# Optimization experiments

Hardware: AMD Instinct MI355X
Metric: run time of the kernel (lower is better)

## Reference

```python
import jax, jax.numpy as jnp
import numpy as np
import math

H = 8  # num_heads

def setup_inputs() -> dict:
    key = jax.random.key(0)
    ks = jax.random.split(key, 12)
    B, N, M, k = 2, 8192, 8192, 32
    dq, dk, dv = 256, 256, 256
    s = 1.0 / math.sqrt(dq)
    inp = {
        'Q': jax.random.normal(ks[0], (B, N, dq), dtype=jnp.float32),
        'K': jax.random.normal(ks[1], (B, M, dk), dtype=jnp.float32),
        'neighbours': jax.random.randint(ks[2], (B, N, k), 0, M),
        'Wq': jax.random.normal(ks[3], (dq, dv), dtype=jnp.float32) * s,
        'bq': jnp.zeros((dv,), dtype=jnp.float32),
        'Wk': jax.random.normal(ks[4], (dk, dv), dtype=jnp.float32) * s,
        'bk': jnp.zeros((dv,), dtype=jnp.float32),
        'Wv': jax.random.normal(ks[5], (dk, dv), dtype=jnp.float32) * s,
        'bv': jnp.zeros((dv,), dtype=jnp.float32),
        'Wo': jax.random.normal(ks[6], (dv, dv), dtype=jnp.float32) * (1.0 / math.sqrt(dv)),
        'bo': jnp.zeros((dv,), dtype=jnp.float32),
    }
    return inp

def reference(Q, K, neighbours, Wq, bq, Wk, bk, Wv, bv, Wo, bo):
    B, N, _ = Q.shape
    dv = Wq.shape[1]
    ds = dv // H
    # project and split heads (contiguous channel chunks == reshape)
    Qh = (Q @ Wq + bq).reshape(B, N, H, ds)            # [B,N,H,ds]
    Kh = (K @ Wk + bk).reshape(B, -1, H, ds)           # [B,M,H,ds]
    Vh = (K @ Wv + bv).reshape(B, -1, H, ds)           # [B,M,H,ds]
    # gather per-node kNN neighbour keys/values: [B,N,k,H,ds]
    gather = jax.vmap(lambda x, idx: x[idx])
    Kn = gather(Kh, neighbours)
    Vn = gather(Vh, neighbours)
    # scale uses full latent size (faithful to original), not head dim
    scale = 1.0 / math.sqrt(dv)
    E = jnp.einsum('bnhd,bnkhd->bnhk', Qh, Kn) * scale  # [B,N,H,k]
    A = jax.nn.softmax(E, axis=-1)
    AV = jnp.einsum('bnhk,bnkhd->bnhd', A, Vn).reshape(B, N, dv)
    return AV @ Wo + bo
```

## Files before the change

kernel.cpp:

```cpp
#include <hip/hip_runtime.h>
#include <hip/hip_bf16.h>
#include <stdint.h>

typedef unsigned short u16;
typedef __attribute__((ext_vector_type(8))) short short8;
typedef __attribute__((ext_vector_type(4))) float f32x4;

__device__ __forceinline__ u16 f2bf(float f) {
    union { float f; unsigned int i; } v; v.f = f;
    unsigned int b = v.i;
    return (u16)((b + 0x7FFFu + ((b >> 16) & 1u)) >> 16);
}

__device__ __forceinline__ short8 cvt8(float4 a, float4 b) {
    union { __hip_bfloat162 h[4]; short8 s; } u;
    u.h[0] = __float22bfloat162_rn(make_float2(a.x, a.y));
    u.h[1] = __float22bfloat162_rn(make_float2(a.z, a.w));
    u.h[2] = __float22bfloat162_rn(make_float2(b.x, b.y));
    u.h[3] = __float22bfloat162_rn(make_float2(b.z, b.w));
    return u.s;
}

typedef const __attribute__((address_space(1))) void* as1cv;
typedef __attribute__((address_space(3))) void* as3v;
__device__ __forceinline__ void gload16(const void* g, void* l) {
    __builtin_amdgcn_global_load_lds((as1cv)g, (as3v)l, 16, 0, 0);
}

__device__ __forceinline__ void up2(unsigned int v, float& lo, float& hi) {
    union { unsigned int i; float f; } a, b;
    a.i = v << 16; b.i = v & 0xffff0000u;
    lo = a.f; hi = b.f;
}

__global__ __launch_bounds__(256) void wprep(
    const float* __restrict__ W0, const float* __restrict__ W1,
    const float* __restrict__ W2, const float* __restrict__ W3,
    u16* __restrict__ T0, u16* __restrict__ T1,
    u16* __restrict__ T2, u16* __restrict__ T3)
{
    const float* W = blockIdx.z == 0 ? W0 : blockIdx.z == 1 ? W1 : blockIdx.z == 2 ? W2 : W3;
    u16*        T  = blockIdx.z == 0 ? T0 : blockIdx.z == 1 ? T1 : blockIdx.z == 2 ? T2 : T3;
    __shared__ u16 ts[64][65];
    int k0 = blockIdx.x * 64, n0 = blockIdx.y * 64;
    int t = threadIdx.x;
    int r = t >> 2, cq = (t & 3) * 16;
    const float4* src = reinterpret_cast<const float4*>(W + (k0 + r) * 256 + n0 + cq);
    for (int u = 0; u < 4; ++u) {
        float4 v = src[u];
        int c = cq + u * 4;
        ts[r][c + 0] = f2bf(v.x); ts[r][c + 1] = f2bf(v.y);
        ts[r][c + 2] = f2bf(v.z); ts[r][c + 3] = f2bf(v.w);
    }
    __syncthreads();
    u16* dst = T + (n0 + r) * 256 + k0 + cq;
    for (int u = 0; u < 16; ++u) dst[u] = ts[cq + u][r];
}

__global__ __launch_bounds__(256) void gemm_proj(
    const float* __restrict__ Q, const float* __restrict__ K,
    const u16* __restrict__ Wtq, const u16* __restrict__ Wtk, const u16* __restrict__ Wtv,
    const float* __restrict__ bq, const float* __restrict__ bk, const float* __restrict__ bv,
    u16* __restrict__ Qh, u16* __restrict__ Kh, u16* __restrict__ Vh)
{
    int z = blockIdx.z;
    const float* Af   = (z == 0) ? Q   : K;
    const u16*   Wt   = (z == 0) ? Wtq : (z == 1) ? Wtk : Wtv;
    const float* bias = (z == 0) ? bq  : (z == 1) ? bk  : bv;
    u16*         C    = (z == 0) ? Qh  : (z == 1) ? Kh  : Vh;

    __shared__ float Asf[128 * 64];
    __shared__ u16   Bs[128 * 64];

    int t = threadIdx.x;
    int lane = t & 63, w = t >> 6;
    int row0 = blockIdx.x * 128, col0 = blockIdx.y * 128;
    int wr = (w >> 1) * 64, wc = (w & 1) * 64;
    int qd = lane >> 4, md = lane & 15;

    f32x4 acc[4][4] = {};

    for (int kt = 0; kt < 256; kt += 64) {
#pragma unroll
        for (int u = 0; u < 8; ++u) {
            int chunk = w * 8 + u;
            int s = chunk * 64 + lane;
            int r = s >> 4, c = s & 15;
            gload16(Af + (size_t)(row0 + r) * 256 + kt + ((c ^ (r & 15)) * 4),
                    (char*)Asf + chunk * 1024);
        }
#pragma unroll
        for (int u = 0; u < 4; ++u) {
            int chunk = w * 4 + u;
            int s = chunk * 64 + lane;
            int r = s >> 3, c = s & 7;
            gload16(Wt + (size_t)(col0 + r) * 256 + kt + ((c ^ (r & 7)) * 8),
                    (char*)Bs + chunk * 1024);
        }
        __syncthreads();
#pragma unroll
        for (int ks = 0; ks < 64; ks += 32) {
            short8 af[4], bf[4];
#pragma unroll
            for (int i = 0; i < 4; ++i) {
                int ar = wr + i * 16 + md;
                int c0 = (ks >> 2) + qd * 2;
                int x = ar & 15;
                float4 fa0 = reinterpret_cast<const float4*>(Asf)[ar * 16 + (c0 ^ x)];
                float4 fa1 = reinterpret_cast<const float4*>(Asf)[ar * 16 + ((c0 + 1) ^ x)];
                af[i] = cvt8(fa0, fa1);
            }
#pragma unroll
            for (int j = 0; j < 4; ++j) {
                int br = wc + j * 16 + md;
                int slot = ((ks >> 3) + qd) ^ (br & 7);
                bf[j] = reinterpret_cast<const short8*>(Bs)[br * 8 + slot];
            }
#pragma unroll
            for (int i = 0; i < 4; ++i)
#pragma unroll
                for (int j = 0; j < 4; ++j)
                    acc[i][j] = __builtin_amdgcn_mfma_f32_16x16x32_bf16(
                        af[i], bf[j], acc[i][j], 0, 0, 0);
        }
        __syncthreads();
    }

#pragma unroll
    for (int i = 0; i < 4; ++i)
#pragma unroll
        for (int j = 0; j < 4; ++j) {
            int col = col0 + wc + j * 16 + md;
            float b = bias[col];
#pragma unroll
            for (int r = 0; r < 4; ++r) {
                int row = row0 + wr + i * 16 + qd * 4 + r;
                C[(size_t)row * 256 + col] = f2bf(acc[i][j][r] + b);
            }
        }
}

__global__ __launch_bounds__(256) void gemm_out(
    const u16* __restrict__ Ab, const u16* __restrict__ Wt,
    const float* __restrict__ bias, float* __restrict__ Cout)
{
    __shared__ u16 As[64 * 64];
    __shared__ u16 Bs[128 * 64];

    int t = threadIdx.x;
    int lane = t & 63, w = t >> 6;
    int row0 = blockIdx.x * 64, col0 = blockIdx.y * 128;
    int wr = (w >> 1) * 32, wc = (w & 1) * 64;
    int qd = lane >> 4, md = lane & 15;

    f32x4 acc[2][4] = {};

    for (int kt = 0; kt < 256; kt += 64) {
#pragma unroll
        for (int u = 0; u < 2; ++u) {
            int chunk = w * 2 + u;
            int s = chunk * 64 + lane;
            int r = s >> 3, c = s & 7;
            gload16(Ab + (size_t)(row0 + r) * 256 + kt + ((c ^ (r & 7)) * 8),
                    (char*)As + chunk * 1024);
        }
#pragma unroll
        for (int u = 0; u < 4; ++u) {
            int chunk = w * 4 + u;
            int s = chunk * 64 + lane;
            int r = s >> 3, c = s & 7;
            gload16(Wt + (size_t)(col0 + r) * 256 + kt + ((c ^ (r & 7)) * 8),
                    (char*)Bs + chunk * 1024);
        }
        __syncthreads();
#pragma unroll
        for (int ks = 0; ks < 64; ks += 32) {
            short8 af[2], bf[4];
#pragma unroll
            for (int i = 0; i < 2; ++i) {
                int ar = wr + i * 16 + md;
                int slot = ((ks >> 3) + qd) ^ (ar & 7);
                af[i] = reinterpret_cast<const short8*>(As)[ar * 8 + slot];
            }
#pragma unroll
            for (int j = 0; j < 4; ++j) {
                int br = wc + j * 16 + md;
                int slot = ((ks >> 3) + qd) ^ (br & 7);
                bf[j] = reinterpret_cast<const short8*>(Bs)[br * 8 + slot];
            }
#pragma unroll
            for (int i = 0; i < 2; ++i)
#pragma unroll
                for (int j = 0; j < 4; ++j)
                    acc[i][j] = __builtin_amdgcn_mfma_f32_16x16x32_bf16(
                        af[i], bf[j], acc[i][j], 0, 0, 0);
        }
        __syncthreads();
    }

#pragma unroll
    for (int i = 0; i < 2; ++i)
#pragma unroll
        for (int j = 0; j < 4; ++j) {
            int col = col0 + wc + j * 16 + md;
            float b = bias[col];
#pragma unroll
            for (int r = 0; r < 4; ++r) {
                int row = row0 + wr + i * 16 + qd * 4 + r;
                Cout[(size_t)row * 256 + col] = acc[i][j][r] + b;
            }
        }
}

__device__ __forceinline__ int attn_row(int blk, int w) {
    int g = blk & 7;
    int batch = g >> 2;
    int group = (blk >> 3) * 4 + (g & 3);
    return batch * 8192 + group * 4 + w;
}

__global__ __launch_bounds__(256) void attn_score(
    const u16* __restrict__ Qh, const u16* __restrict__ Kh,
    const int* __restrict__ nbr, u16* __restrict__ Wgt)
{
    __shared__ int jbs[4][32];
    __shared__ u16 wsm[4][256];

    int t = threadIdx.x;
    int w = t >> 6, lane = t & 63;
    int row = attn_row(blockIdx.x, w);
    int bbase = (row >> 13) << 13;

    int c8 = lane & 31;
    int jh = lane >> 5;

    if (lane < 32) {
        int ji = nbr[(size_t)row * 32 + lane];
        jbs[w][lane] = (bbase + ji) * 256;
    }

    float qf[8];
    {
        uint4 qw = *reinterpret_cast<const uint4*>(Qh + (size_t)row * 256 + c8 * 8);
        up2(qw.x, qf[0], qf[1]); up2(qw.y, qf[2], qf[3]);
        up2(qw.z, qf[4], qf[5]); up2(qw.w, qf[6], qf[7]);
    }

    float e16[16];
#pragma unroll
    for (int bb = 0; bb < 2; ++bb) {
        uint4 kw[8];
#pragma unroll
        for (int u = 0; u < 8; ++u) {
            int koff = jbs[w][jh * 16 + bb * 8 + u];
            kw[u] = *reinterpret_cast<const uint4*>(Kh + (size_t)koff + c8 * 8);
        }
#pragma unroll
        for (int u = 0; u < 8; ++u) {
            float k0, k1;
            float p = 0.f;
            up2(kw[u].x, k0, k1); p = fmaf(qf[0], k0, p); p = fmaf(qf[1], k1, p);
            up2(kw[u].y, k0, k1); p = fmaf(qf[2], k0, p); p = fmaf(qf[3], k1, p);
            up2(kw[u].z, k0, k1); p = fmaf(qf[4], k0, p); p = fmaf(qf[5], k1, p);
            up2(kw[u].w, k0, k1); p = fmaf(qf[6], k0, p); p = fmaf(qf[7], k1, p);
            p += __shfl_xor(p, 1);
            p += __shfl_xor(p, 2);
            e16[bb * 8 + u] = p * 0.0625f;
        }
    }

    float m = e16[0];
#pragma unroll
    for (int jj = 1; jj < 16; ++jj) m = fmaxf(m, e16[jj]);
    m = fmaxf(m, __shfl_xor(m, 32));
    float s = 0.f;
#pragma unroll
    for (int jj = 0; jj < 16; ++jj) { e16[jj] = __expf(e16[jj] - m); s += e16[jj]; }
    s += __shfl_xor(s, 32);
    float rs = 1.0f / s;

    if ((c8 & 3) == 0) {
        int h = c8 >> 2;
#pragma unroll
        for (int jj = 0; jj < 16; ++jj)
            wsm[w][h * 32 + jh * 16 + jj] = f2bf(e16[jj] * rs);
    }
    __syncthreads();

    {
        uint2 v = *reinterpret_cast<const uint2*>(&wsm[w][lane * 4]);
        *reinterpret_cast<uint2*>(Wgt + (size_t)row * 256 + lane * 4) = v;
    }
}

__global__ __launch_bounds__(256) void attn_av(
    const u16* __restrict__ Vh, const int* __restrict__ nbr,
    const u16* __restrict__ Wgt, u16* __restrict__ AVb)
{
    __shared__ int jbs[4][32];

    int t = threadIdx.x;
    int w = t >> 6, lane = t & 63;
    int row = attn_row(blockIdx.x, w);
    int bbase = (row >> 13) << 13;

    int c8 = lane & 31;
    int jh = lane >> 5;
    int h = c8 >> 2;

    if (lane < 32) {
        int ji = nbr[(size_t)row * 32 + lane];
        jbs[w][lane] = (bbase + ji) * 256;
    }

    float e16[16];
    {
        const uint4* wp = reinterpret_cast<const uint4*>(
            Wgt + (size_t)row * 256 + h * 32 + jh * 16);
        uint4 v = wp[0];
        up2(v.x, e16[0], e16[1]);  up2(v.y, e16[2], e16[3]);
        up2(v.z, e16[4], e16[5]);  up2(v.w, e16[6], e16[7]);
        v = wp[1];
        up2(v.x, e16[8], e16[9]);  up2(v.y, e16[10], e16[11]);
        up2(v.z, e16[12], e16[13]); up2(v.w, e16[14], e16[15]);
    }

    float acc[8] = {};
#pragma unroll
    for (int bb = 0; bb < 2; ++bb) {
        uint4 vv[8];
#pragma unroll
        for (int u = 0; u < 8; ++u) {
            int voff = jbs[w][jh * 16 + bb * 8 + u];
            vv[u] = *reinterpret_cast<const uint4*>(Vh + (size_t)voff + c8 * 8);
        }
#pragma unroll
        for (int u = 0; u < 8; ++u) {
            float v0, v1;
            float wgt = e16[bb * 8 + u];
            up2(vv[u].x, v0, v1); acc[0] = fmaf(wgt, v0, acc[0]); acc[1] = fmaf(wgt, v1, acc[1]);
            up2(vv[u].y, v0, v1); acc[2] = fmaf(wgt, v0, acc[2]); acc[3] = fmaf(wgt, v1, acc[3]);
            up2(vv[u].z, v0, v1); acc[4] = fmaf(wgt, v0, acc[4]); acc[5] = fmaf(wgt, v1, acc[5]);
            up2(vv[u].w, v0, v1); acc[6] = fmaf(wgt, v0, acc[6]); acc[7] = fmaf(wgt, v1, acc[7]);
        }
    }
#pragma unroll
    for (int u = 0; u < 8; ++u) acc[u] += __shfl_xor(acc[u], 32);

    if (lane < 32) {
        union { __hip_bfloat162 h2[4]; uint4 u4; } o;
        o.h2[0] = __float22bfloat162_rn(make_float2(acc[0], acc[1]));
        o.h2[1] = __float22bfloat162_rn(make_float2(acc[2], acc[3]));
        o.h2[2] = __float22bfloat162_rn(make_float2(acc[4], acc[5]));
        o.h2[3] = __float22bfloat162_rn(make_float2(acc[6], acc[7]));
        *reinterpret_cast<uint4*>(AVb + (size_t)row * 256 + c8 * 8) = o.u4;
    }
}

extern "C" void kernel_launch(void* const* d_in, const int* in_sizes, int n_in,
                              void* d_out, int out_size, void* d_ws, size_t ws_size,
                              hipStream_t stream) {
    const float* Q   = (const float*)d_in[0];
    const float* K   = (const float*)d_in[1];
    const int*   nbr = (const int*)d_in[2];
    const float* Wq  = (const float*)d_in[3];
    const float* bq  = (const float*)d_in[4];
    const float* Wk  = (const float*)d_in[5];
    const float* bk  = (const float*)d_in[6];
    const float* Wv  = (const float*)d_in[7];
    const float* bv  = (const float*)d_in[8];
    const float* Wo  = (const float*)d_in[9];
    const float* bo  = (const float*)d_in[10];
    float* out = (float*)d_out;

    char* ws = (char*)d_ws;
    size_t off = 0;
    auto alloc = [&](size_t bytes) -> void* {
        void* p = ws + off;
        off += (bytes + 255) & ~(size_t)255;
        return p;
    };
    const size_t MN = 16384;
    u16* Wtq = (u16*)alloc(256 * 256 * 2);
    u16* Wtk = (u16*)alloc(256 * 256 * 2);
    u16* Wtv = (u16*)alloc(256 * 256 * 2);
    u16* Wto = (u16*)alloc(256 * 256 * 2);
    u16* Qh  = (u16*)alloc(MN * 256 * 2);
    u16* Kh  = (u16*)alloc(MN * 256 * 2);
    u16* Vh  = (u16*)alloc(MN * 256 * 2);
    u16* AVb = (u16*)alloc(MN * 256 * 2);
    u16* Wgt = (u16*)alloc(MN * 256 * 2);

    wprep<<<dim3(4, 4, 4), 256, 0, stream>>>(Wq, Wk, Wv, Wo, Wtq, Wtk, Wtv, Wto);
    gemm_proj<<<dim3(128, 2, 3), 256, 0, stream>>>(Q, K, Wtq, Wtk, Wtv,
                                                   bq, bk, bv, Qh, Kh, Vh);
    attn_score<<<dim3(4096), 256, 0, stream>>>(Qh, Kh, nbr, Wgt);
    attn_av<<<dim3(4096), 256, 0, stream>>>(Vh, nbr, Wgt, AVb);
    gemm_out<<<dim3(256, 2), 256, 0, stream>>>(AVb, Wto, bo, out);
}
```

Before: 152.6 us.

## Retile projection GEMM to full-width columns and split attention rows by head half

The projection GEMM now gives each block 64 rows and all 256 output columns, so the fp32 activation tile is loaded and converted to bf16 once per row block rather than once for each of two column blocks. The attention score and AV kernels now give each wave half of a row's heads (128 channels), doubling the grid. This lowers per-wave register use, lets each wave issue its gathers in one batch, and removes the shared-memory staging and __syncthreads in the score kernel. In exchange there are extra cross-lane shuffle reductions, neighbour indices are loaded twice per row, and the GEMM holds more accumulators per wave.

New measurement: 153.7 us. Within noise of the previous version (+0.7%).

```diff
diff --git a/kernel.cpp b/kernel.cpp
--- a/kernel.cpp
+++ b/kernel.cpp
@@ -69,25 +69,100 @@
     const float* bias = (z == 0) ? bq  : (z == 1) ? bk  : bv;
     u16*         C    = (z == 0) ? Qh  : (z == 1) ? Kh  : Vh;
 
-    __shared__ float Asf[128 * 64];
-    __shared__ u16   Bs[128 * 64];
+    __shared__ float Asf[64 * 64];
+    __shared__ u16   Bs[256 * 64];
 
     int t = threadIdx.x;
     int lane = t & 63, w = t >> 6;
-    int row0 = blockIdx.x * 128, col0 = blockIdx.y * 128;
-    int wr = (w >> 1) * 64, wc = (w & 1) * 64;
+    int row0 = blockIdx.x * 64;
+    int wr = (w >> 1) * 32, wc = (w & 1) * 128;
     int qd = lane >> 4, md = lane & 15;
 
-    f32x4 acc[4][4] = {};
+    f32x4 acc[2][8] = {};
 
     for (int kt = 0; kt < 256; kt += 64) {
 #pragma unroll
-        for (int u = 0; u < 8; ++u) {
-            int chunk = w * 8 + u;
+        for (int u = 0; u < 4; ++u) {
+            int chunk = w * 4 + u;
             int s = chunk * 64 + lane;
             int r = s >> 4, c = s & 15;
             gload16(Af + (size_t)(row0 + r) * 256 + kt + ((c ^ (r & 15)) * 4),
                     (char*)Asf + chunk * 1024);
+        }
+#pragma unroll
+        for (int u = 0; u < 8; ++u) {
+            int chunk = w * 8 + u;
+            int s = chunk * 64 + lane;
+            int r = s >> 3, c = s & 7;
+            gload16(Wt + (size_t)r * 256 + kt + ((c ^ (r & 7)) * 8),
+                    (char*)Bs + chunk * 1024);
+        }
+        __syncthreads();
+#pragma unroll
+        for (int ks = 0; ks < 64; ks += 32) {
+            short8 af[2], bf[8];
+#pragma unroll
+            for (int i = 0; i < 2; ++i) {
+                int ar = wr + i * 16 + md;
+                int c0 = (ks >> 2) + qd * 2;
+                int x = ar & 15;
+                float4 fa0 = reinterpret_cast<const float4*>(Asf)[ar * 16 + (c0 ^ x)];
+                float4 fa1 = reinterpret_cast<const float4*>(Asf)[ar * 16 + ((c0 + 1) ^ x)];
+                af[i] = cvt8(fa0, fa1);
+            }
+#pragma unroll
+            for (int j = 0; j < 8; ++j) {
+                int br = wc + j * 16 + md;
+                int slot = ((ks >> 3) + qd) ^ (br & 7);
+                bf[j] = reinterpret_cast<const short8*>(Bs)[br * 8 + slot];
+            }
+#pragma unroll
+            for (int i = 0; i < 2; ++i)
+#pragma unroll
+                for (int j = 0; j < 8; ++j)
+                    acc[i][j] = __builtin_amdgcn_mfma_f32_16x16x32_bf16(
+                        af[i], bf[j], acc[i][j], 0, 0, 0);
+        }
+        __syncthreads();
+    }
+
+#pragma unroll
+    for (int i = 0; i < 2; ++i)
+#pragma unroll
+        for (int j = 0; j < 8; ++j) {
+            int col = wc + j * 16 + md;
+            float b = bias[col];
+#pragma unroll
+            for (int r = 0; r < 4; ++r) {
+                int row = row0 + wr + i * 16 + qd * 4 + r;
+                C[(size_t)row * 256 + col] = f2bf(acc[i][j][r] + b);
+            }
+        }
+}
+
+__global__ __launch_bounds__(256) void gemm_out(
+    const u16* __restrict__ Ab, const u16* __restrict__ Wt,
+    const float* __restrict__ bias, float* __restrict__ Cout)
+{
+    __shared__ u16 As[64 * 64];
+    __shared__ u16 Bs[128 * 64];
+
+    int t = threadIdx.x;
+    int lane = t & 63, w = t >> 6;
+    int row0 = blockIdx.x * 64, col0 = blockIdx.y * 128;
+    int wr = (w >> 1) * 32, wc = (w & 1) * 64;
+    int qd = lane >> 4, md = lane & 15;
+
+    f32x4 acc[2][4] = {};
+
+    for (int kt = 0; kt < 256; kt += 64) {
+#pragma unroll
+        for (int u = 0; u < 2; ++u) {
+            int chunk = w * 2 + u;
+            int s = chunk * 64 + lane;
+            int r = s >> 3, c = s & 7;
+            gload16(Ab + (size_t)(row0 + r) * 256 + kt + ((c ^ (r & 7)) * 8),
+                    (char*)As + chunk * 1024);
         }
 #pragma unroll
         for (int u = 0; u < 4; ++u) {
@@ -100,15 +175,12 @@
         __syncthreads();
 #pragma unroll
         for (int ks = 0; ks < 64; ks += 32) {
-            short8 af[4], bf[4];
-#pragma unroll
-            for (int i = 0; i < 4; ++i) {
+            short8 af[2], bf[4];
+#pragma unroll
+            for (int i = 0; i < 2; ++i) {
                 int ar = wr + i * 16 + md;
-                int c0 = (ks >> 2) + qd * 2;
-                int x = ar & 15;
-                float4 fa0 = reinterpret_cast<const float4*>(Asf)[ar * 16 + (c0 ^ x)];
-                float4 fa1 = reinterpret_cast<const float4*>(Asf)[ar * 16 + ((c0 + 1) ^ x)];
-                af[i] = cvt8(fa0, fa1);
+                int slot = ((ks >> 3) + qd) ^ (ar & 7);
+                af[i] = reinterpret_cast<const short8*>(As)[ar * 8 + slot];
             }
 #pragma unroll
             for (int j = 0; j < 4; ++j) {
@@ -117,7 +189,7 @@
                 bf[j] = reinterpret_cast<const short8*>(Bs)[br * 8 + slot];
             }
 #pragma unroll
-            for (int i = 0; i < 4; ++i)
+            for (int i = 0; i < 2; ++i)
 #pragma unroll
                 for (int j = 0; j < 4; ++j)
                     acc[i][j] = __builtin_amdgcn_mfma_f32_16x16x32_bf16(
@@ -127,7 +199,7 @@
     }
 
 #pragma unroll
-    for (int i = 0; i < 4; ++i)
+    for (int i = 0; i < 2; ++i)
 #pragma unroll
         for (int j = 0; j < 4; ++j) {
             int col = col0 + wc + j * 16 + md;
@@ -135,88 +207,17 @@
 #pragma unroll
             for (int r = 0; r < 4; ++r) {
                 int row = row0 + wr + i * 16 + qd * 4 + r;
-                C[(size_t)row * 256 + col] = f2bf(acc[i][j][r] + b);
-            }
-        }
-}
-
-__global__ __launch_bounds__(256) void gemm_out(
-    const u16* __restrict__ Ab, const u16* __restrict__ Wt,
-    const float* __restrict__ bias, float* __restrict__ Cout)
-{
-    __shared__ u16 As[64 * 64];
-    __shared__ u16 Bs[128 * 64];
-
-    int t = threadIdx.x;
-    int lane = t & 63, w = t >> 6;
-    int row0 = blockIdx.x * 64, col0 = blockIdx.y * 128;
-    int wr = (w >> 1) * 32, wc = (w & 1) * 64;
-    int qd = lane >> 4, md = lane & 15;
-
-    f32x4 acc[2][4] = {};
-
-    for (int kt = 0; kt < 256; kt += 64) {
-#pragma unroll
-        for (int u = 0; u < 2; ++u) {
-            int chunk = w * 2 + u;
-            int s = chunk * 64 + lane;
-            int r = s >> 3, c = s & 7;
-            gload16(Ab + (size_t)(row0 + r) * 256 + kt + ((c ^ (r & 7)) * 8),
-                    (char*)As + chunk * 1024);
-        }
-#pragma unroll
-        for (int u = 0; u < 4; ++u) {
-            int chunk = w * 4 + u;
-            int s = chunk * 64 + lane;
-            int r = s >> 3, c = s & 7;
-            gload16(Wt + (size_t)(col0 + r) * 256 + kt + ((c ^ (r & 7)) * 8),
-                    (char*)Bs + chunk * 1024);
-        }
-        __syncthreads();
-#pragma unroll
-        for (int ks = 0; ks < 64; ks += 32) {
-            short8 af[2], bf[4];
-#pragma unroll
-            for (int i = 0; i < 2; ++i) {
-                int ar = wr + i * 16 + md;
-                int slot = ((ks >> 3) + qd) ^ (ar & 7);
-                af[i] = reinterpret_cast<const short8*>(As)[ar * 8 + slot];
-            }
-#pragma unroll
-            for (int j = 0; j < 4; ++j) {
-                int br = wc + j * 16 + md;
-                int slot = ((ks >> 3) + qd) ^ (br & 7);
-                bf[j] = reinterpret_cast<const short8*>(Bs)[br * 8 + slot];
-            }
-#pragma unroll
-            for (int i = 0; i < 2; ++i)
-#pragma unroll
-                for (int j = 0; j < 4; ++j)
-                    acc[i][j] = __builtin_amdgcn_mfma_f32_16x16x32_bf16(
-                        af[i], bf[j], acc[i][j], 0, 0, 0);
-        }
-        __syncthreads();
-    }
-
-#pragma unroll
-    for (int i = 0; i < 2; ++i)
-#pragma unroll
-        for (int j = 0; j < 4; ++j) {
-            int col = col0 + wc + j * 16 + md;
-            float b = bias[col];
-#pragma unroll
-            for (int r = 0; r < 4; ++r) {
-                int row = row0 + wr + i * 16 + qd * 4 + r;
                 Cout[(size_t)row * 256 + col] = acc[i][j][r] + b;
             }
         }
 }
 
-__device__ __forceinline__ int attn_row(int blk, int w) {
+__device__ __forceinline__ void attn_map2(int blk, int w, int& row, int& hf) {
     int g = blk & 7;
     int batch = g >> 2;
-    int group = (blk >> 3) * 4 + (g & 3);
-    return batch * 8192 + group * 4 + w;
+    hf = (g >> 1) & 1;
+    int cb = (blk >> 3) * 2 + (g & 1);
+    row = batch * 8192 + cb * 4 + w;
 }
 
 __global__ __launch_bounds__(256) void attn_score(
@@ -224,72 +225,67 @@
     const int* __restrict__ nbr, u16* __restrict__ Wgt)
 {
     __shared__ int jbs[4][32];
-    __shared__ u16 wsm[4][256];
 
     int t = threadIdx.x;
     int w = t >> 6, lane = t & 63;
-    int row = attn_row(blockIdx.x, w);
+    int row, hf;
+    attn_map2(blockIdx.x, w, row, hf);
     int bbase = (row >> 13) << 13;
 
-    int c8 = lane & 31;
-    int jh = lane >> 5;
+    int c4 = lane & 15;
+    int jg = lane >> 4;
 
     if (lane < 32) {
         int ji = nbr[(size_t)row * 32 + lane];
-        jbs[w][lane] = (bbase + ji) * 256;
+        jbs[w][lane] = (bbase + ji) * 256 + hf * 128;
     }
 
     float qf[8];
     {
-        uint4 qw = *reinterpret_cast<const uint4*>(Qh + (size_t)row * 256 + c8 * 8);
+        uint4 qw = *reinterpret_cast<const uint4*>(Qh + (size_t)row * 256 + hf * 128 + c4 * 8);
         up2(qw.x, qf[0], qf[1]); up2(qw.y, qf[2], qf[3]);
         up2(qw.z, qf[4], qf[5]); up2(qw.w, qf[6], qf[7]);
     }
 
-    float e16[16];
-#pragma unroll
-    for (int bb = 0; bb < 2; ++bb) {
-        uint4 kw[8];
-#pragma unroll
-        for (int u = 0; u < 8; ++u) {
-            int koff = jbs[w][jh * 16 + bb * 8 + u];
-            kw[u] = *reinterpret_cast<const uint4*>(Kh + (size_t)koff + c8 * 8);
-        }
-#pragma unroll
-        for (int u = 0; u < 8; ++u) {
-            float k0, k1;
-            float p = 0.f;
-            up2(kw[u].x, k0, k1); p = fmaf(qf[0], k0, p); p = fmaf(qf[1], k1, p);
-            up2(kw[u].y, k0, k1); p = fmaf(qf[2], k0, p); p = fmaf(qf[3], k1, p);
-            up2(kw[u].z, k0, k1); p = fmaf(qf[4], k0, p); p = fmaf(qf[5], k1, p);
-            up2(kw[u].w, k0, k1); p = fmaf(qf[6], k0, p); p = fmaf(qf[7], k1, p);
-            p += __shfl_xor(p, 1);
-            p += __shfl_xor(p, 2);
-            e16[bb * 8 + u] = p * 0.0625f;
-        }
-    }
-
-    float m = e16[0];
-#pragma unroll
-    for (int jj = 1; jj < 16; ++jj) m = fmaxf(m, e16[jj]);
+    uint4 kw[8];
+#pragma unroll
+    for (int u = 0; u < 8; ++u) {
+        int koff = jbs[w][jg * 8 + u];
+        kw[u] = *reinterpret_cast<const uint4*>(Kh + (size_t)koff + c4 * 8);
+    }
+
+    float e8[8];
+#pragma unroll
+    for (int u = 0; u < 8; ++u) {
+        float k0, k1;
+        float p = 0.f;
+        up2(kw[u].x, k0, k1); p = fmaf(qf[0], k0, p); p = fmaf(qf[1], k1, p);
+        up2(kw[u].y, k0, k1); p = fmaf(qf[2], k0, p); p = fmaf(qf[3], k1, p);
+        up2(kw[u].z, k0, k1); p = fmaf(qf[4], k0, p); p = fmaf(qf[5], k1, p);
+        up2(kw[u].w, k0, k1); p = fmaf(qf[6], k0, p); p = fmaf(qf[7], k1, p);
+        p += __shfl_xor(p, 1);
+        p += __shfl_xor(p, 2);
+        e8[u] = p * 0.0625f;
+    }
+
+    float m = e8[0];
+#pragma unroll
+    for (int jj = 1; jj < 8; ++jj) m = fmaxf(m, e8[jj]);
+    m = fmaxf(m, __shfl_xor(m, 16));
     m = fmaxf(m, __shfl_xor(m, 32));
     float s = 0.f;
 #pragma unroll
-    for (int jj = 0; jj < 16; ++jj) { e16[jj] = __expf(e16[jj] - m); s += e16[jj]; }
+    for (int jj = 0; jj < 8; ++jj) { e8[jj] = __expf(e8[jj] - m); s += e8[jj]; }
+    s += __shfl_xor(s, 16);
     s += __shfl_xor(s, 32);
     float rs = 1.0f / s;
 
-    if ((c8 & 3) == 0) {
-        int h = c8 >> 2;
-#pragma unroll
-        for (int jj = 0; jj < 16; ++jj)
-            wsm[w][h * 32 + jh * 16 + jj] = f2bf(e16[jj] * rs);
-    }
-    __syncthreads();
-
-    {
-        uint2 v = *reinterpret_cast<const uint2*>(&wsm[w][lane * 4]);
-        *reinterpret_cast<uint2*>(Wgt + (size_t)row * 256 + lane * 4) = v;
+    if ((c4 & 3) == 0) {
+        int hh = c4 >> 2;
+        union { u16 h[8]; uint4 u4; } o;
+#pragma unroll
+        for (int jj = 0; jj < 8; ++jj) o.h[jj] = f2bf(e8[jj] * rs);
+        *reinterpret_cast<uint4*>(Wgt + (size_t)row * 256 + (hf * 4 + hh) * 32 + jg * 8) = o.u4;
     }
 }
 
@@ -301,59 +297,57 @@
 
     int t = threadIdx.x;
     int w = t >> 6, lane = t & 63;
-    int row = attn_row(blockIdx.x, w);
+    int row, hf;
+    attn_map2(blockIdx.x, w, row, hf);
     int bbase = (row >> 13) << 13;
 
-    int c8 = lane & 31;
-    int jh = lane >> 5;
-    int h = c8 >> 2;
+    int c4 = lane & 15;
+    int jg = lane >> 4;
+    int hh = c4 >> 2;
 
     if (lane < 32) {
         int ji = nbr[(size_t)row * 32 + lane];
-        jbs[w][lane] = (bbase + ji) * 256;
-    }
-
-    float e16[16];
+        jbs[w][lane] = (bbase + ji) * 256 + hf * 128;
+    }
+
+    float e8[8];
     {
-        const uint4* wp = reinterpret_cast<const uint4*>(
-            Wgt + (size_t)row * 256 + h * 32 + jh * 16);
-        uint4 v = wp[0];
-        up2(v.x, e16[0], e16[1]);  up2(v.y, e16[2], e16[3]);
-        up2(v.z, e16[4], e16[5]);  up2(v.w, e16[6], e16[7]);
-        v = wp[1];
-        up2(v.x, e16[8], e16[9]);  up2(v.y, e16[10], e16[11]);
-        up2(v.z, e16[12], e16[13]); up2(v.w, e16[14], e16[15]);
+        uint4 v = *reinterpret_cast<const uint4*>(
+            Wgt + (size_t)row * 256 + (hf * 4 + hh) * 32 + jg * 8);
+        up2(v.x, e8[0], e8[1]); up2(v.y, e8[2], e8[3]);
+        up2(v.z, e8[4], e8[5]); up2(v.w, e8[6], e8[7]);
+    }
+
+    uint4 vv[8];
+#pragma unroll
+    for (int u = 0; u < 8; ++u) {
+        int voff = jbs[w][jg * 8 + u];
+        vv[u] = *reinterpret_cast<const uint4*>(Vh + (size_t)voff + c4 * 8);
     }
 
     float acc[8] = {};
 #pragma unroll
-    for (int bb = 0; bb < 2; ++bb) {
-        uint4 vv[8];
-#pragma unroll
-        for (int u = 0; u < 8; ++u) {
-            int voff = jbs[w][jh * 16 + bb * 8 + u];
-            vv[u] = *reinterpret_cast<const uint4*>(Vh + (size_t)voff + c8 * 8);
-        }
-#pragma unroll
-        for (int u = 0; u < 8; ++u) {
-            float v0, v1;
-            float wgt = e16[bb * 8 + u];
-            up2(vv[u].x, v0, v1); acc[0] = fmaf(wgt, v0, acc[0]); acc[1] = fmaf(wgt, v1, acc[1]);
-            up2(vv[u].y, v0, v1); acc[2] = fmaf(wgt, v0, acc[2]); acc[3] = fmaf(wgt, v1, acc[3]);
-            up2(vv[u].z, v0, v1); acc[4] = fmaf(wgt, v0, acc[4]); acc[5] = fmaf(wgt, v1, acc[5]);
-            up2(vv[u].w, v0, v1); acc[6] = fmaf(wgt, v0, acc[6]); acc[7] = fmaf(wgt, v1, acc[7]);
-        }
-    }
-#pragma unroll
-    for (int u = 0; u < 8; ++u) acc[u] += __shfl_xor(acc[u], 32);
-
-    if (lane < 32) {
+    for (int u = 0; u < 8; ++u) {
+        float v0, v1;
+        float wgt = e8[u];
+        up2(vv[u].x, v0, v1); acc[0] = fmaf(wgt, v0, acc[0]); acc[1] = fmaf(wgt, v1, acc[1]);
+        up2(vv[u].y, v0, v1); acc[2] = fmaf(wgt, v0, acc[2]); acc[3] = fmaf(wgt, v1, acc[3]);
+        up2(vv[u].z, v0, v1); acc[4] = fmaf(wgt, v0, acc[4]); acc[5] = fmaf(wgt, v1, acc[5]);
+        up2(vv[u].w, v0, v1); acc[6] = fmaf(wgt, v0, acc[6]); acc[7] = fmaf(wgt, v1, acc[7]);
+    }
+#pragma unroll
+    for (int u = 0; u < 8; ++u) {
+        acc[u] += __shfl_xor(acc[u], 16);
+        acc[u] += __shfl_xor(acc[u], 32);
+    }
+
+    if (lane < 16) {
         union { __hip_bfloat162 h2[4]; uint4 u4; } o;
         o.h2[0] = __float22bfloat162_rn(make_float2(acc[0], acc[1]));
         o.h2[1] = __float22bfloat162_rn(make_float2(acc[2], acc[3]));
         o.h2[2] = __float22bfloat162_rn(make_float2(acc[4], acc[5]));
         o.h2[3] = __float22bfloat162_rn(make_float2(acc[6], acc[7]));
-        *reinterpret_cast<uint4*>(AVb + (size_t)row * 256 + c8 * 8) = o.u4;
+        *reinterpret_cast<uint4*>(AVb + (size_t)row * 256 + hf * 128 + c4 * 8) = o.u4;
     }
 }
 
@@ -392,9 +386,9 @@
     u16* Wgt = (u16*)alloc(MN * 256 * 2);
 
     wprep<<<dim3(4, 4, 4), 256, 0, stream>>>(Wq, Wk, Wv, Wo, Wtq, Wtk, Wtv, Wto);
-    gemm_proj<<<dim3(128, 2, 3), 256, 0, stream>>>(Q, K, Wtq, Wtk, Wtv,
+    gemm_proj<<<dim3(256, 1, 3), 256, 0, stream>>>(Q, K, Wtq, Wtk, Wtv,
                                                    bq, bk, bv, Qh, Kh, Vh);
-    attn_score<<<dim3(4096), 256, 0, stream>>>(Qh, Kh, nbr, Wgt);
-    attn_av<<<dim3(4096), 256, 0, stream>>>(Vh, nbr, Wgt, AVb);
+    attn_score<<<dim3(8192), 256, 0, stream>>>(Qh, Kh, nbr, Wgt);
+    attn_av<<<dim3(8192), 256, 0, stream>>>(Vh, nbr, Wgt, AVb);
     gemm_out<<<dim3(256, 2), 256, 0, stream>>>(AVb, Wto, bo, out);
 }
```
